# Kernel optimization log

Hardware: AMD Instinct MI355X
Metric: run time of the kernel (lower is better)

The kernel has to match this reference:

```python
import jax, jax.numpy as jnp
import numpy as np

K = 3  # kernel_size
PAD = 1  # floor(K/2) * padding

@jax.custom_vjp
def sign_ste(x):
    # Binarize to {-1, 0, +1}; straight-through (identity) gradient, matching
    # the .data-based binarization / normal-conv backward of the original.
    return jnp.sign(x)

def _sign_fwd(x):
    return jnp.sign(x), None

def _sign_bwd(_, g):
    return (g,)

sign_ste.defvjp(_sign_fwd, _sign_bwd)


def setup_inputs() -> dict:
    key = jax.random.key(0)
    k1, k2 = jax.random.split(key)
    b, c_in, h, w = 8, 128, 16, 16
    c_out = 128
    x = jax.random.normal(k1, (b, c_in, h, w), dtype=jnp.float32)
    stdv = 1.0 / np.sqrt(c_in * K * K)
    weight = jax.random.uniform(k2, (c_out, K, K, c_in), dtype=jnp.float32,
                                minval=-stdv, maxval=stdv)
    return {"x": x, "weight": weight}


def reference(x, weight):
    # x: (b, c_in, H, W) NCHW.  weight: (c_out, K, K, c_in).
    # c_in != 3 -> binarize input; weight is always binarized.
    xb = sign_ste(x)
    wb = sign_ste(weight)

    # NCHW -> NHWC (the CUDA kernel operates on NHWC)
    x_nhwc = jnp.transpose(xb, (0, 2, 3, 1))
    b, H, W, c_in = x_nhwc.shape

    # zero padding: padded taps contribute 0 to the 3-way partial sums
    xp = jnp.pad(x_nhwc, ((0, 0), (PAD, PAD), (PAD, PAD), (0, 0)))

    # patches: (b, H, W, Ky, Kx, c_in)  -- K*K = 9 static shifted views
    patches = jnp.stack(
        [jnp.stack([xp[:, ky:ky + H, kx:kx + W, :] for kx in range(K)], axis=3)
         for ky in range(K)], axis=3)

    # Maj3: XNOR products of a kernel row (3 taps along Kx) are summed,
    # the majority of each triple is its sign, then majorities are
    # accumulated over kernel rows and input channels (approx popcount).
    # partial sums over the 3 kx taps per (ky, c_in): (b,H,W,Ky,c_out,c_in)
    s = jnp.einsum('bhwyxc,oyxc->bhwyoc', patches, wb)
    m = sign_ste(s)                      # majority of each 3-input group
    out = jnp.sum(m, axis=(3, 5))        # sum over Ky and c_in -> (b,H,W,c_out)
    return jnp.transpose(out, (0, 3, 1, 2))  # back to NCHW
```

## Files before the change

### kernel.cpp

```cpp
#include <hip/hip_runtime.h>
#include <stdint.h>

#define B    8
#define CIN  128
#define H    16
#define W    16
#define COUT 128

__global__ void pack_signs_kernel(const float* __restrict__ x,
                                  const float* __restrict__ wgt,
                                  unsigned long long* __restrict__ xb,
                                  unsigned long long* __restrict__ wb) {
    const int NX = B * H * W * CIN;
    const int NW = COUT * 9 * CIN;
    int tid = blockIdx.x * blockDim.x + threadIdx.x;
    if (tid < NX) {
        int c   = tid & 127;
        int pos = tid >> 7;
        int w = pos & 15, h = (pos >> 4) & 15, b = pos >> 8;
        float v = x[((b * CIN + c) * H + h) * W + w];
        unsigned long long m = __ballot(v > 0.0f);
        if ((threadIdx.x & 63) == 0) xb[pos * 2 + (c >> 6)] = m;
    } else if (tid < NX + NW) {
        int idx = tid - NX;
        int c   = idx & 127;
        int pos = idx >> 7;
        float v = wgt[pos * 128 + c];
        unsigned long long m = __ballot(v > 0.0f);
        if ((threadIdx.x & 63) == 0) wb[pos * 2 + (c >> 6)] = m;
    }
}

__global__ __launch_bounds__(256) void maj3_kernel(
        const unsigned long long* __restrict__ xb,
        const unsigned long long* __restrict__ wb,
        float* __restrict__ out) {
    const int bo = blockIdx.x;
    const int o  = bo & 127;
    const int b  = bo >> 7;
    const int h  = threadIdx.x >> 4;
    const int w  = threadIdx.x & 15;

    __shared__ unsigned long long sx[H * W * 2];
    {
        int i = threadIdx.x;
        sx[i * 2]     = xb[(b * 256 + i) * 2];
        sx[i * 2 + 1] = xb[(b * 256 + i) * 2 + 1];
    }
    __syncthreads();

    unsigned long long wreg[9][2];
#pragma unroll
    for (int k = 0; k < 9; ++k) {
        wreg[k][0] = wb[(o * 9 + k) * 2];
        wreg[k][1] = wb[(o * 9 + k) * 2 + 1];
    }

    int acc = 0;
#pragma unroll
    for (int ky = 0; ky < 3; ++ky) {
        int ih = h + ky - 1;
        if (ih < 0 || ih >= H) continue;

        unsigned long long p[3][2];
        bool v0 = (w - 1 >= 0);
        bool v2 = (w + 1 < W);
#pragma unroll
        for (int kx = 0; kx < 3; ++kx) {
            int iw = w + kx - 1;
            int iwc = iw < 0 ? 0 : (iw > W - 1 ? W - 1 : iw);
            int base = (ih * W + iwc) * 2;
            p[kx][0] = ~(sx[base]     ^ wreg[ky * 3 + kx][0]);
            p[kx][1] = ~(sx[base + 1] ^ wreg[ky * 3 + kx][1]);
        }
        if (v0 && v2) {
            unsigned long long m0 = (p[0][0] & p[1][0]) | ((p[0][0] | p[1][0]) & p[2][0]);
            unsigned long long m1 = (p[0][1] & p[1][1]) | ((p[0][1] | p[1][1]) & p[2][1]);
            acc += 2 * (__popcll(m0) + __popcll(m1)) - 128;
        } else {
            unsigned long long q0 = v0 ? p[0][0] : p[2][0];
            unsigned long long q1 = v0 ? p[0][1] : p[2][1];
            acc += __popcll(p[1][0] & q0) + __popcll(p[1][1] & q1)
                 + __popcll(p[1][0] | q0) + __popcll(p[1][1] | q1) - 128;
        }
    }
    out[((b * COUT + o) * H + h) * W + w] = (float)acc;
}

extern "C" void kernel_launch(void* const* d_in, const int* in_sizes, int n_in,
                              void* d_out, int out_size, void* d_ws, size_t ws_size,
                              hipStream_t stream) {
    const float* x   = (const float*)d_in[0];
    const float* wgt = (const float*)d_in[1];
    float* out = (float*)d_out;

    unsigned long long* xb = (unsigned long long*)d_ws;
    unsigned long long* wb = (unsigned long long*)((char*)d_ws + 32768);

    const int NPACK = B * H * W * CIN + COUT * 9 * CIN;
    pack_signs_kernel<<<NPACK / 256, 256, 0, stream>>>(x, wgt, xb, wb);
    maj3_kernel<<<B * COUT, 256, 0, stream>>>(xb, wb, out);
}
```

Baseline: 12.98 us.

## Fuse sign packing into maj3 kernel and compute four output channels per block

Removes the separate pack kernel and the workspace round trip by having each block binarize its own batch image and four output channels' weights directly into shared memory. Each block of 512 threads computes 4 output channels (2 per thread) and reuses the loaded input bits across channels, cutting the launch count to one with 256 blocks. The cost is redundant input packing: each batch image is re-read and re-packed by 32 blocks, and each thread does 64 strided loads serially to build its mask.

```diff
diff --git a/kernel.cpp b/kernel.cpp
--- a/kernel.cpp
+++ b/kernel.cpp
@@ -7,84 +7,88 @@
 #define W    16
 #define COUT 128
 
-__global__ void pack_signs_kernel(const float* __restrict__ x,
-                                  const float* __restrict__ wgt,
-                                  unsigned long long* __restrict__ xb,
-                                  unsigned long long* __restrict__ wb) {
-    const int NX = B * H * W * CIN;
-    const int NW = COUT * 9 * CIN;
-    int tid = blockIdx.x * blockDim.x + threadIdx.x;
-    if (tid < NX) {
-        int c   = tid & 127;
-        int pos = tid >> 7;
-        int w = pos & 15, h = (pos >> 4) & 15, b = pos >> 8;
-        float v = x[((b * CIN + c) * H + h) * W + w];
-        unsigned long long m = __ballot(v > 0.0f);
-        if ((threadIdx.x & 63) == 0) xb[pos * 2 + (c >> 6)] = m;
-    } else if (tid < NX + NW) {
-        int idx = tid - NX;
-        int c   = idx & 127;
-        int pos = idx >> 7;
-        float v = wgt[pos * 128 + c];
-        unsigned long long m = __ballot(v > 0.0f);
-        if ((threadIdx.x & 63) == 0) wb[pos * 2 + (c >> 6)] = m;
+__global__ __launch_bounds__(512) void maj3_fused_kernel(
+        const float* __restrict__ x,
+        const float* __restrict__ wgt,
+        float* __restrict__ out) {
+    const int blk = blockIdx.x;
+    const int og  = blk & 31;
+    const int b   = blk >> 5;
+    const int t   = threadIdx.x;
+
+    __shared__ unsigned long long sx[16 * 17 * 2];
+    __shared__ unsigned long long sw[4 * 9 * 2];
+
+    {
+        const int wave = t >> 6, lane = t & 63;
+        #pragma unroll
+        for (int j = 0; j < 9; ++j) {
+            int i    = wave * 9 + j;
+            int word = i & 1;
+            int k    = (i >> 1) % 9;
+            int ol   = (i >> 1) / 9;
+            float v = wgt[(((og * 4 + ol) * 9 + k) << 7) + (word << 6) + lane];
+            unsigned long long m = __ballot(v > 0.0f);
+            if (lane == 0) sw[i] = m;
+        }
     }
-}
 
-__global__ __launch_bounds__(256) void maj3_kernel(
-        const unsigned long long* __restrict__ xb,
-        const unsigned long long* __restrict__ wb,
-        float* __restrict__ out) {
-    const int bo = blockIdx.x;
-    const int o  = bo & 127;
-    const int b  = bo >> 7;
-    const int h  = threadIdx.x >> 4;
-    const int w  = threadIdx.x & 15;
-
-    __shared__ unsigned long long sx[H * W * 2];
     {
-        int i = threadIdx.x;
-        sx[i * 2]     = xb[(b * 256 + i) * 2];
-        sx[i * 2 + 1] = xb[(b * 256 + i) * 2 + 1];
+        const int word = t >> 8;
+        const int pos  = t & 255;
+        const float* xp = x + ((b * CIN + (word << 6)) << 8) + pos;
+        unsigned long long m = 0;
+        #pragma unroll
+        for (int j = 0; j < 64; ++j)
+            m |= (unsigned long long)(xp[j << 8] > 0.0f) << j;
+        int h = pos >> 4, w = pos & 15;
+        sx[(h * 17 + w) * 2 + word] = m;
     }
     __syncthreads();
 
-    unsigned long long wreg[9][2];
-#pragma unroll
-    for (int k = 0; k < 9; ++k) {
-        wreg[k][0] = wb[(o * 9 + k) * 2];
-        wreg[k][1] = wb[(o * 9 + k) * 2 + 1];
-    }
+    const int pos   = t & 255;
+    const int opair = t >> 8;
+    const int h = pos >> 4, w = pos & 15;
+    const bool v0 = (w > 0), v2 = (w < 15);
+    int acc0 = 0, acc1 = 0;
 
-    int acc = 0;
-#pragma unroll
+    #pragma unroll
     for (int ky = 0; ky < 3; ++ky) {
         int ih = h + ky - 1;
         if (ih < 0 || ih >= H) continue;
 
-        unsigned long long p[3][2];
-        bool v0 = (w - 1 >= 0);
-        bool v2 = (w + 1 < W);
-#pragma unroll
-        for (int kx = 0; kx < 3; ++kx) {
-            int iw = w + kx - 1;
-            int iwc = iw < 0 ? 0 : (iw > W - 1 ? W - 1 : iw);
-            int base = (ih * W + iwc) * 2;
-            p[kx][0] = ~(sx[base]     ^ wreg[ky * 3 + kx][0]);
-            p[kx][1] = ~(sx[base + 1] ^ wreg[ky * 3 + kx][1]);
-        }
-        if (v0 && v2) {
-            unsigned long long m0 = (p[0][0] & p[1][0]) | ((p[0][0] | p[1][0]) & p[2][0]);
-            unsigned long long m1 = (p[0][1] & p[1][1]) | ((p[0][1] | p[1][1]) & p[2][1]);
-            acc += 2 * (__popcll(m0) + __popcll(m1)) - 128;
-        } else {
-            unsigned long long q0 = v0 ? p[0][0] : p[2][0];
-            unsigned long long q1 = v0 ? p[0][1] : p[2][1];
-            acc += __popcll(p[1][0] & q0) + __popcll(p[1][1] & q1)
-                 + __popcll(p[1][0] | q0) + __popcll(p[1][1] | q1) - 128;
+        int base = ih * 17 * 2;
+        int iwl = v0 ? (w - 1) : w;
+        int iwr = v2 ? (w + 1) : w;
+        unsigned long long s00 = sx[base + iwl * 2], s01 = sx[base + iwl * 2 + 1];
+        unsigned long long s10 = sx[base + w   * 2], s11 = sx[base + w   * 2 + 1];
+        unsigned long long s20 = sx[base + iwr * 2], s21 = sx[base + iwr * 2 + 1];
+
+        #pragma unroll
+        for (int oo = 0; oo < 2; ++oo) {
+            int ol = opair * 2 + oo;
+            const unsigned long long* wk = &sw[(ol * 9 + ky * 3) * 2];
+            unsigned long long p00 = ~(s00 ^ wk[0]), p01 = ~(s01 ^ wk[1]);
+            unsigned long long p10 = ~(s10 ^ wk[2]), p11 = ~(s11 ^ wk[3]);
+            unsigned long long p20 = ~(s20 ^ wk[4]), p21 = ~(s21 ^ wk[5]);
+            int a;
+            if (v0 && v2) {
+                unsigned long long m0 = (p00 & p10) | ((p00 | p10) & p20);
+                unsigned long long m1 = (p01 & p11) | ((p01 | p11) & p21);
+                a = 2 * (__popcll(m0) + __popcll(m1)) - 128;
+            } else {
+                unsigned long long q0 = v0 ? p00 : p20;
+                unsigned long long q1 = v0 ? p01 : p21;
+                a = __popcll(p10 & q0) + __popcll(p11 & q1)
+                  + __popcll(p10 | q0) + __popcll(p11 | q1) - 128;
+            }
+            if (oo == 0) acc0 += a; else acc1 += a;
         }
     }
-    out[((b * COUT + o) * H + h) * W + w] = (float)acc;
+
+    const int o0 = og * 4 + opair * 2;
+    out[((b * COUT + o0) << 8) + pos]       = (float)acc0;
+    out[((b * COUT + o0 + 1) << 8) + pos]   = (float)acc1;
 }
 
 extern "C" void kernel_launch(void* const* d_in, const int* in_sizes, int n_in,
@@ -94,10 +98,5 @@
     const float* wgt = (const float*)d_in[1];
     float* out = (float*)d_out;
 
-    unsigned long long* xb = (unsigned long long*)d_ws;
-    unsigned long long* wb = (unsigned long long*)((char*)d_ws + 32768);
-
-    const int NPACK = B * H * W * CIN + COUT * 9 * CIN;
-    pack_signs_kernel<<<NPACK / 256, 256, 0, stream>>>(x, wgt, xb, wb);
-    maj3_kernel<<<B * COUT, 256, 0, stream>>>(xb, wb, out);
+    maj3_fused_kernel<<<B * (COUT / 4), 512, 0, stream>>>(x, wgt, out);
 }
```

Measured after the change: 10.91 us. -16.0%, faster.
